# Kernel optimization log

Measured on AMD Instinct MI355X. Metric: run time of the kernel, lower is better.

## Reference

```python
import jax, jax.numpy as jnp
import numpy as np

N = 50000
HEADS1, HIM = 8, 16
NEG_SLOPE = 0.2


def gat_conv(x, src, dst, W, a_src, a_dst, bias, heads, out_dim, concat):
    n = x.shape[0]
    h = (x @ W).reshape(n, heads, out_dim)                      # [N,H,D]
    al_src = jnp.einsum('nhd,hd->nh', h, a_src)                  # [N,H]
    al_dst = jnp.einsum('nhd,hd->nh', h, a_dst)                  # [N,H]
    e = jax.nn.leaky_relu(al_src[src] + al_dst[dst], NEG_SLOPE)  # [E,H]
    # segment softmax over incoming edges of each destination node
    e_max = jax.ops.segment_max(e, dst, num_segments=n)
    e_max = jnp.where(jnp.isfinite(e_max), e_max, 0.0)
    ex = jnp.exp(e - e_max[dst])
    denom = jax.ops.segment_sum(ex, dst, num_segments=n)
    denom = jnp.where(denom == 0.0, 1.0, denom)
    alpha = ex / denom[dst]                                      # [E,H]
    msg = h[src] * alpha[:, :, None]                             # [E,H,D]
    out = jax.ops.segment_sum(msg, dst, num_segments=n)          # [N,H,D]
    out = out.reshape(n, heads * out_dim) if concat else out.mean(axis=1)
    return out + bias


def setup_inputs() -> dict:
    key = jax.random.key(0)
    ks = jax.random.split(key, 12)
    num_feature, out_feature, him = 128, 121, HIM
    E = 800000
    x = jax.random.normal(ks[0], (N, num_feature), dtype=jnp.float32)
    edge_index = jax.random.randint(ks[1], (2, E), 0, N, dtype=jnp.int64)
    s = 0.1
    W1 = jax.random.normal(ks[2], (num_feature, HEADS1 * him), dtype=jnp.float32) * s
    a_src1 = jax.random.normal(ks[3], (HEADS1, him), dtype=jnp.float32) * s
    a_dst1 = jax.random.normal(ks[4], (HEADS1, him), dtype=jnp.float32) * s
    b1 = jnp.zeros((HEADS1 * him,), dtype=jnp.float32)
    W2 = jax.random.normal(ks[5], (HEADS1 * him, out_feature), dtype=jnp.float32) * s
    a_src2 = jax.random.normal(ks[6], (1, out_feature), dtype=jnp.float32) * s
    a_dst2 = jax.random.normal(ks[7], (1, out_feature), dtype=jnp.float32) * s
    b2 = jnp.zeros((out_feature,), dtype=jnp.float32)
    return {"x": x, "edge_index": edge_index, "W1": W1, "a_src1": a_src1,
            "a_dst1": a_dst1, "b1": b1, "W2": W2, "a_src2": a_src2,
            "a_dst2": a_dst2, "b2": b2}


def reference(x, edge_index, W1, a_src1, a_dst1, b1, W2, a_src2, a_dst2, b2):
    n = x.shape[0]
    loops = jnp.arange(n, dtype=edge_index.dtype)
    src = jnp.concatenate([edge_index[0], loops])  # add self-loops (PyG default)
    dst = jnp.concatenate([edge_index[1], loops])
    h = gat_conv(x, src, dst, W1, a_src1, a_dst1, b1, HEADS1, HIM, True)
    h = jax.nn.relu(h)
    out = gat_conv(h, src, dst, W2, a_src2, a_dst2, b2, 1, W2.shape[1], True)
    return out
```

## Files before the change

kernel.cpp:

```cpp
#include <hip/hip_runtime.h>
#include <hip/hip_fp16.h>

#define NEG_SLOPE 0.2f

typedef __fp16 half8v __attribute__((ext_vector_type(8)));
typedef __fp16 half4v __attribute__((ext_vector_type(4)));
typedef float f32x4 __attribute__((ext_vector_type(4)));
typedef unsigned uint4u __attribute__((ext_vector_type(4), aligned(4)));
typedef float f32x4u __attribute__((ext_vector_type(4), aligned(4)));

__device__ __forceinline__ float lrelu(float x) {
    return fmaxf(x, 0.0f) + NEG_SLOPE * fminf(x, 0.0f);
}

__device__ __forceinline__ unsigned fkey(float f) {
    unsigned u = __float_as_uint(f);
    return (u & 0x80000000u) ? ~u : (u | 0x80000000u);
}
__device__ __forceinline__ float funkey(unsigned k) {
    return __uint_as_float((k & 0x80000000u) ? (k & 0x7fffffffu) : ~k);
}


__global__ __launch_bounds__(256) void scan_reduce(const int* __restrict__ cnt,
                                                   int* __restrict__ bsum, int n) {
    __shared__ int sm[256];
    int base = blockIdx.x * 1024 + threadIdx.x * 4;
    int s = 0;
#pragma unroll
    for (int j = 0; j < 4; ++j) {
        int i = base + j;
        if (i < n) s += cnt[i];
    }
    sm[threadIdx.x] = s;
    __syncthreads();
#pragma unroll
    for (int off = 128; off >= 1; off >>= 1) {
        if (threadIdx.x < off) sm[threadIdx.x] += sm[threadIdx.x + off];
        __syncthreads();
    }
    if (threadIdx.x == 0) bsum[blockIdx.x] = sm[0];
}

__global__ __launch_bounds__(256) void scan_bsum256(int* __restrict__ bsum, int nb) {
    __shared__ int sm[256];
    int v = (threadIdx.x < (unsigned)nb) ? bsum[threadIdx.x] : 0;
    sm[threadIdx.x] = v;
    __syncthreads();
    for (int off = 1; off < 256; off <<= 1) {
        int y = (threadIdx.x >= off) ? sm[threadIdx.x - off] : 0;
        __syncthreads();
        sm[threadIdx.x] += y;
        __syncthreads();
    }
    if (threadIdx.x < (unsigned)nb) bsum[threadIdx.x] = sm[threadIdx.x] - v;
}

__global__ __launch_bounds__(256) void scan_write(const int* __restrict__ cnt,
                                                  const int* __restrict__ bsum,
                                                  int* __restrict__ rp, int n) {
    __shared__ int sm[256];
    int base = blockIdx.x * 1024 + threadIdx.x * 4;
    int v[4];
    int s = 0;
#pragma unroll
    for (int j = 0; j < 4; ++j) {
        int i = base + j;
        v[j] = (i < n) ? cnt[i] : 0;
        s += v[j];
    }
    sm[threadIdx.x] = s;
    __syncthreads();
#pragma unroll
    for (int off = 1; off < 256; off <<= 1) {
        int y = (threadIdx.x >= off) ? sm[threadIdx.x - off] : 0;
        __syncthreads();
        sm[threadIdx.x] += y;
        __syncthreads();
    }
    int run = sm[threadIdx.x] - s + bsum[blockIdx.x];
#pragma unroll
    for (int j = 0; j < 4; ++j) {
        int i = base + j;
        if (i < n) {
            rp[i] = run;
            run += v[j];
            if (i == n - 1) rp[n] = run;
        }
    }
}


__global__ __launch_bounds__(256) void rhist1_kernel(const int* __restrict__ dst,
                                                     int* __restrict__ h, int E, int nblk) {
    __shared__ int lh[256];
    lh[threadIdx.x] = 0;
    __syncthreads();
    int base = blockIdx.x * 1024;
#pragma unroll
    for (int j = 0; j < 4; ++j) {
        int i = base + j * 256 + threadIdx.x;
        if (i < E) atomicAdd(&lh[dst[i] & 255], 1);
    }
    __syncthreads();
    h[threadIdx.x * nblk + blockIdx.x] = lh[threadIdx.x];
}

__global__ __launch_bounds__(256) void rhist2_kernel(const unsigned* __restrict__ kv,
                                                     int* __restrict__ h, int E, int nblk) {
    __shared__ int lh[256];
    lh[threadIdx.x] = 0;
    __syncthreads();
    int base = blockIdx.x * 1024;
#pragma unroll
    for (int j = 0; j < 4; ++j) {
        int i = base + j * 256 + threadIdx.x;
        if (i < E) atomicAdd(&lh[kv[i] >> 24], 1);
    }
    __syncthreads();
    h[threadIdx.x * nblk + blockIdx.x] = lh[threadIdx.x];
}

template <int SH, bool PACK>
__global__ __launch_bounds__(256) void rscat_kernel(const unsigned* __restrict__ in,
                                                    const int* __restrict__ srcp,
                                                    const int* __restrict__ dstp,
                                                    unsigned* __restrict__ outv,
                                                    const int* __restrict__ scanned,
                                                    int E, int nblk) {
    __shared__ unsigned items[1024];
    __shared__ unsigned sorted[1024];
    __shared__ int lh[256], lstart[256], rbase[256];
    __shared__ int wcnt[4][256];

    int tid = threadIdx.x, blk = blockIdx.x;
    int base = blk * 1024;
    int k = min(1024, E - base);
    lh[tid] = 0;
    rbase[tid] = 0;
#pragma unroll
    for (int j = 0; j < 4; ++j) {
        int idx = j * 256 + tid;
        unsigned v = 0u;
        if (base + idx < E) {
            if constexpr (PACK)
                v = ((unsigned)dstp[base + idx] << 16) | (unsigned)srcp[base + idx];
            else
                v = in[base + idx];
        }
        items[idx] = v;
    }
    __syncthreads();
#pragma unroll
    for (int j = 0; j < 4; ++j) {
        int idx = j * 256 + tid;
        if (idx < k) atomicAdd(&lh[(items[idx] >> SH) & 255], 1);
    }
    __syncthreads();
    int sv = lh[tid];
    lstart[tid] = sv;
    __syncthreads();
    for (int off = 1; off < 256; off <<= 1) {
        int y = (tid >= off) ? lstart[tid - off] : 0;
        __syncthreads();
        lstart[tid] += y;
        __syncthreads();
    }
    int excl = lstart[tid] - sv;
    __syncthreads();
    lstart[tid] = excl;
    __syncthreads();

    int lane = tid & 63, wave = tid >> 6;
#pragma unroll
    for (int it = 0; it < 4; ++it) {
        int idx = it * 256 + tid;
        unsigned v = items[idx];
        int d = (v >> SH) & 255;
        bool valid = idx < k;
        unsigned long long m = __ballot(valid);
#pragma unroll
        for (int b = 0; b < 8; ++b) {
            unsigned long long bb = __ballot((d >> b) & 1);
            m &= ((d >> b) & 1) ? bb : ~bb;
        }
        int lanerank = __popcll(m & ((1ull << lane) - 1ull));
        int wtot = __popcll(m);
        wcnt[0][tid] = 0; wcnt[1][tid] = 0; wcnt[2][tid] = 0; wcnt[3][tid] = 0;
        __syncthreads();
        if (valid && lanerank == 0) wcnt[wave][d] = wtot;
        __syncthreads();
        if (valid) {
            int cw = 0;
            for (int w = 0; w < wave; ++w) cw += wcnt[w][d];
            sorted[lstart[d] + rbase[d] + cw + lanerank] = v;
        }
        __syncthreads();
        rbase[tid] += wcnt[0][tid] + wcnt[1][tid] + wcnt[2][tid] + wcnt[3][tid];
        __syncthreads();
    }
#pragma unroll
    for (int j = 0; j < 4; ++j) {
        int i = j * 256 + tid;
        if (i < k) {
            unsigned v = sorted[i];
            int d = (v >> SH) & 255;
            outv[scanned[d * nblk + blk] + (i - lstart[d])] = v;
        }
    }
}


__global__ void rp_kernel(const unsigned* __restrict__ kv, int* __restrict__ rp,
                          int E, int N) {
    int i = blockIdx.x * 256 + threadIdx.x;
    if (i >= E) return;
    int cur = (int)(kv[i] >> 16);
    int prev = (i == 0) ? -1 : (int)(kv[i - 1] >> 16);
    for (int t = prev + 1; t <= cur; ++t) rp[t] = i;
    if (i == E - 1)
        for (int t = cur + 1; t <= N; ++t) rp[t] = E;
}


template <int H>
__global__ __launch_bounds__(256) void gmax_kernel(const float* __restrict__ a,
                                                   unsigned* __restrict__ gm, int total) {
    __shared__ unsigned sm[256];
    unsigned loc = 0;
    int stride = 256 * gridDim.x;
    for (int i = blockIdx.x * 256 + threadIdx.x; i < total; i += stride)
        loc = max(loc, fkey(a[i]));
    sm[threadIdx.x] = loc;
    __syncthreads();
    for (int off = 128; off >= H; off >>= 1) {
        if (threadIdx.x < off) sm[threadIdx.x] = max(sm[threadIdx.x], sm[threadIdx.x + off]);
        __syncthreads();
    }
    if (threadIdx.x < H) atomicMax(&gm[threadIdx.x], sm[threadIdx.x]);
}


__global__ __launch_bounds__(256) void w1_kernel(const unsigned* __restrict__ kv,
                                                 const float* __restrict__ alS,
                                                 const float* __restrict__ alD,
                                                 const unsigned* __restrict__ gm,
                                                 __half* __restrict__ w1t, int E) {
    int e = blockIdx.x * 256 + threadIdx.x;
    if (e >= E) return;
    unsigned k = kv[e];
    int s = (int)(k & 0xFFFFu), t = (int)(k >> 16);
    float sv[8], dv[8];
    *(f32x4*)&sv[0] = *(const f32x4*)(alS + (size_t)s * 8);
    *(f32x4*)&sv[4] = *(const f32x4*)(alS + (size_t)s * 8 + 4);
    *(f32x4*)&dv[0] = *(const f32x4*)(alD + (size_t)t * 8);
    *(f32x4*)&dv[4] = *(const f32x4*)(alD + (size_t)t * 8 + 4);
#pragma unroll
    for (int h = 0; h < 8; ++h) {
        float m = lrelu(funkey(gm[h]) + dv[h]);
        w1t[(size_t)h * E + e] = __float2half(__expf(lrelu(sv[h] + dv[h]) - m));
    }
}

__global__ void w2_kernel(const unsigned* __restrict__ kv, const float* __restrict__ alS,
                          const float* __restrict__ alD, const unsigned* __restrict__ gm,
                          float* __restrict__ w2v, int E) {
    int e = blockIdx.x * 256 + threadIdx.x;
    if (e >= E) return;
    unsigned k = kv[e];
    int s = (int)(k & 0xFFFFu), t = (int)(k >> 16);
    float adT = alD[t];
    w2v[e] = __expf(lrelu(alS[s] + adT) - lrelu(funkey(gm[0]) + adT));
}


template <int NC, typename AT, bool FUSE_AL2>
__global__ __launch_bounds__(256) void gemm_mfma(const AT* __restrict__ A,
                                                 const float* __restrict__ B,
                                                 __half* __restrict__ C, int M,
                                                 const float* __restrict__ as,
                                                 const float* __restrict__ ad,
                                                 float* __restrict__ alS,
                                                 float* __restrict__ alD) {
    __shared__ __half Bt[128][136];

    {
        int t = threadIdx.x;
        int c = t & 127;
        int kq = t >> 7;
#pragma unroll
        for (int ch = 0; ch < 8; ++ch) {
            int k0 = kq * 64 + ch * 8;
            half8v hv;
#pragma unroll
            for (int j = 0; j < 8; ++j) {
                float v = (c < NC) ? B[(size_t)(k0 + j) * NC + c] : 0.0f;
                hv[j] = (__fp16)v;
            }
            *(half8v*)&Bt[c][k0] = hv;
        }
    }
    __syncthreads();

    const int wid = threadIdx.x >> 6;
    const int lane = threadIdx.x & 63;
    const int li = lane & 15;
    const int lg = lane >> 4;

    int row = blockIdx.x * 64 + wid * 16 + li;
    int rowc = min(row, M - 1);

    half8v a[4];
#pragma unroll
    for (int ks = 0; ks < 4; ++ks) {
        int q = ks * 4 + lg;
        if constexpr (sizeof(AT) == 2) {
            a[ks] = *((const half8v*)(A + (size_t)rowc * 128) + q);
        } else {
            const float4* p = (const float4*)(A + (size_t)rowc * 128) + 2 * q;
            float4 a0 = p[0], a1 = p[1];
            half8v hv;
            hv[0] = (__fp16)a0.x; hv[1] = (__fp16)a0.y; hv[2] = (__fp16)a0.z; hv[3] = (__fp16)a0.w;
            hv[4] = (__fp16)a1.x; hv[5] = (__fp16)a1.y; hv[6] = (__fp16)a1.z; hv[7] = (__fp16)a1.w;
            a[ks] = hv;
        }
    }

    f32x4 acc[8];
#pragma unroll
    for (int ct = 0; ct < 8; ++ct) acc[ct] = (f32x4)0.0f;

#pragma unroll
    for (int ks = 0; ks < 4; ++ks) {
#pragma unroll
        for (int ct = 0; ct < 8; ++ct) {
            half8v b = *(const half8v*)&Bt[ct * 16 + li][ks * 32 + 8 * lg];
            acc[ct] = __builtin_amdgcn_mfma_f32_16x16x32_f16(a[ks], b, acc[ct], 0, 0, 0);
        }
    }

    int orow = blockIdx.x * 64 + wid * 16 + 4 * lg;
#pragma unroll
    for (int ct = 0; ct < 8; ++ct) {
#pragma unroll
        for (int r = 0; r < 4; ++r) {
            int rr = orow + r;
            if (rr < M) C[(size_t)rr * 128 + ct * 16 + li] = __float2half(acc[ct][r]);
        }
    }

    if constexpr (FUSE_AL2) {
        float asv[8], adv[8];
#pragma unroll
        for (int ct = 0; ct < 8; ++ct) {
            int c = ct * 16 + li;
            asv[ct] = (c < NC) ? as[c] : 0.0f;
            adv[ct] = (c < NC) ? ad[c] : 0.0f;
        }
#pragma unroll
        for (int r = 0; r < 4; ++r) {
            float s = 0.f, d = 0.f;
#pragma unroll
            for (int ct = 0; ct < 8; ++ct) {
                s = fmaf(acc[ct][r], asv[ct], s);
                d = fmaf(acc[ct][r], adv[ct], d);
            }
            s += __shfl_down(s, 8); d += __shfl_down(d, 8);
            s += __shfl_down(s, 4); d += __shfl_down(d, 4);
            s += __shfl_down(s, 2); d += __shfl_down(d, 2);
            s += __shfl_down(s, 1); d += __shfl_down(d, 1);
            if (li == 0) {
                int rr = orow + r;
                if (rr < M) { alS[rr] = s; alD[rr] = d; }
            }
        }
    }
}


__global__ void al1_kernel(const __half* __restrict__ h1h, const float* __restrict__ as,
                           const float* __restrict__ ad, float* __restrict__ alS,
                           float* __restrict__ alD, int N) {
    int g = blockIdx.x * 256 + threadIdx.x;
    if (g >= N * 8) return;
    int r = g >> 3, h = g & 7;
    const __half2* hp = (const __half2*)(h1h + (size_t)r * 128 + h * 16);
    const float* sp = as + h * 16;
    const float* dp = ad + h * 16;
    float s = 0.f, d = 0.f;
#pragma unroll
    for (int q = 0; q < 8; ++q) {
        float2 v = __half22float2(hp[q]);
        s = fmaf(v.x, sp[2 * q], s);
        d = fmaf(v.x, dp[2 * q], d);
        s = fmaf(v.y, sp[2 * q + 1], s);
        d = fmaf(v.y, dp[2 * q + 1], d);
    }
    alS[g] = s;
    alD[g] = d;
}


__global__ __launch_bounds__(256) void agg1_kernel(
    const __half* __restrict__ h1h, const float* __restrict__ alS,
    const float* __restrict__ alD, const float* __restrict__ b1,
    const int* __restrict__ rp, const unsigned* __restrict__ kv,
    const __half* __restrict__ w1t, const unsigned* __restrict__ gm,
    __half* __restrict__ h2h, int N, int E) {
    int t = blockIdx.x * 4 + (threadIdx.x >> 6);
    int lane = threadIdx.x & 63;
    int h = lane >> 3;

    float adh = alD[t * 8 + h];
    float mh = lrelu(funkey(gm[h]) + adh);
    int e0 = rp[t], e1 = rp[t + 1];

    float ex = __expf(lrelu(alS[t * 8 + h] + adh) - mh);
    float dsum = ex, dsum2 = 0.f;
    float2 hs = __half22float2(*(const __half2*)(h1h + (size_t)t * 128 + 2 * lane));
    float fx = ex * hs.x, fy = ex * hs.y;
    const __half* wrow = w1t + (size_t)h * E;

    int e = e0;
    while (e < e1 && (e & 3)) {
        int s0 = (int)(kv[e] & 0xFFFFu);
        float w0 = __half2float(wrow[e]);
        float2 f0 = __half22float2(*(const __half2*)(h1h + (size_t)s0 * 128 + 2 * lane));
        dsum2 += w0;
        fx = fmaf(w0, f0.x, fx); fy = fmaf(w0, f0.y, fy);
        ++e;
    }
    for (; e + 16 <= e1; e += 16) {
        uint4u kk[4];
        float ww[16];
#pragma unroll
        for (int q = 0; q < 4; ++q) {
            kk[q] = *(const uint4u*)&kv[e + 4 * q];
            half4v wv = *(const half4v*)&wrow[e + 4 * q];
#pragma unroll
            for (int r = 0; r < 4; ++r) ww[q * 4 + r] = (float)wv[r];
        }
        float2 ff[16];
#pragma unroll
        for (int q = 0; q < 4; ++q)
#pragma unroll
            for (int r = 0; r < 4; ++r)
                ff[q * 4 + r] = __half22float2(
                    *(const __half2*)(h1h + (size_t)(kk[q][r] & 0xFFFFu) * 128 + 2 * lane));
#pragma unroll
        for (int q = 0; q < 4; ++q) {
            if (q & 1) dsum2 += (ww[q * 4] + ww[q * 4 + 1]) + (ww[q * 4 + 2] + ww[q * 4 + 3]);
            else       dsum  += (ww[q * 4] + ww[q * 4 + 1]) + (ww[q * 4 + 2] + ww[q * 4 + 3]);
#pragma unroll
            for (int r = 0; r < 4; ++r) {
                float w = ww[q * 4 + r];
                float2 f = ff[q * 4 + r];
                fx = fmaf(w, f.x, fx);
                fy = fmaf(w, f.y, fy);
            }
        }
    }
    if (e + 8 <= e1) {
        uint4u ka = *(const uint4u*)&kv[e];
        uint4u kb = *(const uint4u*)&kv[e + 4];
        half4v wva = *(const half4v*)&wrow[e];
        half4v wvb = *(const half4v*)&wrow[e + 4];
        float2 f0 = __half22float2(*(const __half2*)(h1h + (size_t)(ka.x & 0xFFFFu) * 128 + 2 * lane));
        float2 f1 = __half22float2(*(const __half2*)(h1h + (size_t)(ka.y & 0xFFFFu) * 128 + 2 * lane));
        float2 f2 = __half22float2(*(const __half2*)(h1h + (size_t)(ka.z & 0xFFFFu) * 128 + 2 * lane));
        float2 f3 = __half22float2(*(const __half2*)(h1h + (size_t)(ka.w & 0xFFFFu) * 128 + 2 * lane));
        float2 f4 = __half22float2(*(const __half2*)(h1h + (size_t)(kb.x & 0xFFFFu) * 128 + 2 * lane));
        float2 f5 = __half22float2(*(const __half2*)(h1h + (size_t)(kb.y & 0xFFFFu) * 128 + 2 * lane));
        float2 f6 = __half22float2(*(const __half2*)(h1h + (size_t)(kb.z & 0xFFFFu) * 128 + 2 * lane));
        float2 f7 = __half22float2(*(const __half2*)(h1h + (size_t)(kb.w & 0xFFFFu) * 128 + 2 * lane));
        float w0 = (float)wva[0], w1 = (float)wva[1], w2 = (float)wva[2], w3 = (float)wva[3];
        float w4 = (float)wvb[0], w5 = (float)wvb[1], w6 = (float)wvb[2], w7 = (float)wvb[3];
        dsum += (w0 + w1) + (w2 + w3);
        dsum2 += (w4 + w5) + (w6 + w7);
        fx = fmaf(w0, f0.x, fx); fy = fmaf(w0, f0.y, fy);
        fx = fmaf(w1, f1.x, fx); fy = fmaf(w1, f1.y, fy);
        fx = fmaf(w2, f2.x, fx); fy = fmaf(w2, f2.y, fy);
        fx = fmaf(w3, f3.x, fx); fy = fmaf(w3, f3.y, fy);
        fx = fmaf(w4, f4.x, fx); fy = fmaf(w4, f4.y, fy);
        fx = fmaf(w5, f5.x, fx); fy = fmaf(w5, f5.y, fy);
        fx = fmaf(w6, f6.x, fx); fy = fmaf(w6, f6.y, fy);
        fx = fmaf(w7, f7.x, fx); fy = fmaf(w7, f7.y, fy);
        e += 8;
    }
    if (e + 4 <= e1) {
        uint4u ka = *(const uint4u*)&kv[e];
        half4v wva = *(const half4v*)&wrow[e];
        float2 f0 = __half22float2(*(const __half2*)(h1h + (size_t)(ka.x & 0xFFFFu) * 128 + 2 * lane));
        float2 f1 = __half22float2(*(const __half2*)(h1h + (size_t)(ka.y & 0xFFFFu) * 128 + 2 * lane));
        float2 f2 = __half22float2(*(const __half2*)(h1h + (size_t)(ka.z & 0xFFFFu) * 128 + 2 * lane));
        float2 f3 = __half22float2(*(const __half2*)(h1h + (size_t)(ka.w & 0xFFFFu) * 128 + 2 * lane));
        float w0 = (float)wva[0], w1 = (float)wva[1], w2 = (float)wva[2], w3 = (float)wva[3];
        dsum += (w0 + w1) + (w2 + w3);
        fx = fmaf(w0, f0.x, fx); fy = fmaf(w0, f0.y, fy);
        fx = fmaf(w1, f1.x, fx); fy = fmaf(w1, f1.y, fy);
        fx = fmaf(w2, f2.x, fx); fy = fmaf(w2, f2.y, fy);
        fx = fmaf(w3, f3.x, fx); fy = fmaf(w3, f3.y, fy);
        e += 4;
    }
    for (; e < e1; ++e) {
        int s0 = (int)(kv[e] & 0xFFFFu);
        float w0 = __half2float(wrow[e]);
        float2 f0 = __half22float2(*(const __half2*)(h1h + (size_t)s0 * 128 + 2 * lane));
        dsum2 += w0;
        fx = fmaf(w0, f0.x, fx); fy = fmaf(w0, f0.y, fy);
    }
    dsum += dsum2;
    float inv = 1.0f / dsum;
    float2 bb = *(const float2*)(b1 + 2 * lane);
    float ox = fmaxf(fmaf(fx, inv, bb.x), 0.0f);
    float oy = fmaxf(fmaf(fy, inv, bb.y), 0.0f);
    *(__half2*)(h2h + (size_t)t * 128 + 2 * lane) = __floats2half2_rn(ox, oy);
}


__global__ __launch_bounds__(256) void agg2_kernel(
    const __half* __restrict__ h3h, const float* __restrict__ alS,
    const float* __restrict__ alD, const float* __restrict__ b2,
    const int* __restrict__ rp, const unsigned* __restrict__ kv,
    const float* __restrict__ w2v, const unsigned* __restrict__ gm,
    float* __restrict__ out, int N, int NC) {
    int t = blockIdx.x * 4 + (threadIdx.x >> 6);
    int lane = threadIdx.x & 63;

    float adT = alD[t];
    float m = lrelu(funkey(gm[0]) + adT);
    int e0 = rp[t], e1 = rp[t + 1];

    float ex = __expf(lrelu(alS[t] + adT) - m);
    float dsum = ex, dsum2 = 0.f;
    float2 hs = __half22float2(*(const __half2*)(h3h + (size_t)t * 128 + 2 * lane));
    float fx = ex * hs.x, fy = ex * hs.y;

    int e = e0;
    for (; e + 16 <= e1; e += 16) {
        uint4u kk[4];
        f32x4u ww[4];
#pragma unroll
        for (int q = 0; q < 4; ++q) {
            kk[q] = *(const uint4u*)&kv[e + 4 * q];
            ww[q] = *(const f32x4u*)&w2v[e + 4 * q];
        }
        float2 ff[16];
#pragma unroll
        for (int q = 0; q < 4; ++q)
#pragma unroll
            for (int r = 0; r < 4; ++r)
                ff[q * 4 + r] = __half22float2(
                    *(const __half2*)(h3h + (size_t)(kk[q][r] & 0xFFFFu) * 128 + 2 * lane));
#pragma unroll
        for (int q = 0; q < 4; ++q) {
            if (q & 1) dsum2 += (ww[q][0] + ww[q][1]) + (ww[q][2] + ww[q][3]);
            else       dsum  += (ww[q][0] + ww[q][1]) + (ww[q][2] + ww[q][3]);
#pragma unroll
            for (int r = 0; r < 4; ++r) {
                float w = ww[q][r];
                float2 f = ff[q * 4 + r];
                fx = fmaf(w, f.x, fx);
                fy = fmaf(w, f.y, fy);
            }
        }
    }
    if (e + 8 <= e1) {
        uint4u ka = *(const uint4u*)&kv[e];
        uint4u kb = *(const uint4u*)&kv[e + 4];
        f32x4u wa = *(const f32x4u*)&w2v[e];
        f32x4u wb = *(const f32x4u*)&w2v[e + 4];
        float2 f0 = __half22float2(*(const __half2*)(h3h + (size_t)(ka.x & 0xFFFFu) * 128 + 2 * lane));
        float2 f1 = __half22float2(*(const __half2*)(h3h + (size_t)(ka.y & 0xFFFFu) * 128 + 2 * lane));
        float2 f2 = __half22float2(*(const __half2*)(h3h + (size_t)(ka.z & 0xFFFFu) * 128 + 2 * lane));
        float2 f3 = __half22float2(*(const __half2*)(h3h + (size_t)(ka.w & 0xFFFFu) * 128 + 2 * lane));
        float2 f4 = __half22float2(*(const __half2*)(h3h + (size_t)(kb.x & 0xFFFFu) * 128 + 2 * lane));
        float2 f5 = __half22float2(*(const __half2*)(h3h + (size_t)(kb.y & 0xFFFFu) * 128 + 2 * lane));
        float2 f6 = __half22float2(*(const __half2*)(h3h + (size_t)(kb.z & 0xFFFFu) * 128 + 2 * lane));
        float2 f7 = __half22float2(*(const __half2*)(h3h + (size_t)(kb.w & 0xFFFFu) * 128 + 2 * lane));
        dsum += (wa[0] + wa[1]) + (wa[2] + wa[3]);
        dsum2 += (wb[0] + wb[1]) + (wb[2] + wb[3]);
        fx = fmaf(wa[0], f0.x, fx); fy = fmaf(wa[0], f0.y, fy);
        fx = fmaf(wa[1], f1.x, fx); fy = fmaf(wa[1], f1.y, fy);
        fx = fmaf(wa[2], f2.x, fx); fy = fmaf(wa[2], f2.y, fy);
        fx = fmaf(wa[3], f3.x, fx); fy = fmaf(wa[3], f3.y, fy);
        fx = fmaf(wb[0], f4.x, fx); fy = fmaf(wb[0], f4.y, fy);
        fx = fmaf(wb[1], f5.x, fx); fy = fmaf(wb[1], f5.y, fy);
        fx = fmaf(wb[2], f6.x, fx); fy = fmaf(wb[2], f6.y, fy);
        fx = fmaf(wb[3], f7.x, fx); fy = fmaf(wb[3], f7.y, fy);
        e += 8;
    }
    if (e + 4 <= e1) {
        uint4u ka = *(const uint4u*)&kv[e];
        f32x4u wa = *(const f32x4u*)&w2v[e];
        float2 f0 = __half22float2(*(const __half2*)(h3h + (size_t)(ka.x & 0xFFFFu) * 128 + 2 * lane));
        float2 f1 = __half22float2(*(const __half2*)(h3h + (size_t)(ka.y & 0xFFFFu) * 128 + 2 * lane));
        float2 f2 = __half22float2(*(const __half2*)(h3h + (size_t)(ka.z & 0xFFFFu) * 128 + 2 * lane));
        float2 f3 = __half22float2(*(const __half2*)(h3h + (size_t)(ka.w & 0xFFFFu) * 128 + 2 * lane));
        dsum += (wa[0] + wa[1]) + (wa[2] + wa[3]);
        fx = fmaf(wa[0], f0.x, fx); fy = fmaf(wa[0], f0.y, fy);
        fx = fmaf(wa[1], f1.x, fx); fy = fmaf(wa[1], f1.y, fy);
        fx = fmaf(wa[2], f2.x, fx); fy = fmaf(wa[2], f2.y, fy);
        fx = fmaf(wa[3], f3.x, fx); fy = fmaf(wa[3], f3.y, fy);
        e += 4;
    }
    for (; e < e1; ++e) {
        int s0 = (int)(kv[e] & 0xFFFFu);
        float w0 = w2v[e];
        float2 f0 = __half22float2(*(const __half2*)(h3h + (size_t)s0 * 128 + 2 * lane));
        dsum2 += w0;
        fx = fmaf(w0, f0.x, fx); fy = fmaf(w0, f0.y, fy);
    }
    dsum += dsum2;
    float inv = 1.0f / dsum;
    int c0 = 2 * lane, c1 = 2 * lane + 1;
    if (c0 < NC) out[(size_t)t * NC + c0] = fmaf(fx, inv, b2[c0]);
    if (c1 < NC) out[(size_t)t * NC + c1] = fmaf(fy, inv, b2[c1]);
}


extern "C" void kernel_launch(void* const* d_in, const int* in_sizes, int n_in,
                              void* d_out, int out_size, void* d_ws, size_t ws_size,
                              hipStream_t stream) {
    const float* x   = (const float*)d_in[0];
    const int*   ei  = (const int*)d_in[1];
    const float* W1  = (const float*)d_in[2];
    const float* aS1 = (const float*)d_in[3];
    const float* aD1 = (const float*)d_in[4];
    const float* b1  = (const float*)d_in[5];
    const float* W2  = (const float*)d_in[6];
    const float* aS2 = (const float*)d_in[7];
    const float* aD2 = (const float*)d_in[8];
    const float* b2  = (const float*)d_in[9];
    float* out = (float*)d_out;

    const int N = in_sizes[0] / 128;
    const int E = in_sizes[1] / 2;
    const int NC2 = 121;

    const int NBLK = (E + 1023) / 1024;
    const int HN = 256 * NBLK;

    size_t off = 0;
    auto alloc = [&](size_t bytes) {
        size_t o = off;
        off = (off + bytes + 255) & ~(size_t)255;
        return o;
    };
    char* ws = (char*)d_ws;
    unsigned* kv0  = (unsigned*)(ws + alloc((size_t)E * 4));
    unsigned* kv1  = (unsigned*)(ws + alloc((size_t)E * 4));
    int*      h    = (int*)(ws + alloc((size_t)(HN + 1) * 4));
    int*      hs   = (int*)(ws + alloc((size_t)(HN + 1) * 4));
    int*      rp   = (int*)(ws + alloc((size_t)(N + 1) * 4));
    int*      bsum = (int*)(ws + alloc(256 * 4));
    float*    alS1 = (float*)(ws + alloc((size_t)N * 8 * 4));
    float*    alD1 = (float*)(ws + alloc((size_t)N * 8 * 4));
    float*    alS2 = (float*)(ws + alloc((size_t)N * 4));
    float*    alD2 = (float*)(ws + alloc((size_t)N * 4));
    unsigned* gm1  = (unsigned*)(ws + alloc(8 * 4));
    unsigned* gm2  = (unsigned*)(ws + alloc(4));
    __half*   w1t  = (__half*)(ws + alloc((size_t)E * 8 * 2));
    __half*   h1h  = (__half*)(ws + alloc((size_t)N * 128 * 2));
    __half*   h2h  = (__half*)(ws + alloc((size_t)N * 128 * 2));
    __half*   h3h  = h1h;
    float*    w2v  = (float*)kv1;
    if (ws_size < off) return;

    const int* src = ei;
    const int* dst = ei + E;

    hipMemsetAsync(gm1, 0, 8 * 4, stream);
    hipMemsetAsync(gm2, 0, 4, stream);

    int eb = (E + 255) / 256;
    int snb = (HN + 1023) / 1024;

    rhist1_kernel<<<NBLK, 256, 0, stream>>>(dst, h, E, NBLK);
    scan_reduce<<<snb, 256, 0, stream>>>(h, bsum, HN);
    scan_bsum256<<<1, 256, 0, stream>>>(bsum, snb);
    scan_write<<<snb, 256, 0, stream>>>(h, bsum, hs, HN);
    rscat_kernel<16, true><<<NBLK, 256, 0, stream>>>(nullptr, src, dst, kv1, hs, E, NBLK);
    rhist2_kernel<<<NBLK, 256, 0, stream>>>(kv1, h, E, NBLK);
    scan_reduce<<<snb, 256, 0, stream>>>(h, bsum, HN);
    scan_bsum256<<<1, 256, 0, stream>>>(bsum, snb);
    scan_write<<<snb, 256, 0, stream>>>(h, bsum, hs, HN);
    rscat_kernel<24, false><<<NBLK, 256, 0, stream>>>(kv1, nullptr, nullptr, kv0, hs, E, NBLK);
    rp_kernel<<<eb, 256, 0, stream>>>(kv0, rp, E, N);

    int gmb = (N + 63) / 64;
    int ab = (N + 3) / 4;
    gemm_mfma<128, float, false><<<gmb, 256, 0, stream>>>(x, W1, h1h, N,
                                                          nullptr, nullptr, nullptr, nullptr);
    al1_kernel<<<(N * 8 + 255) / 256, 256, 0, stream>>>(h1h, aS1, aD1, alS1, alD1, N);
    gmax_kernel<8><<<128, 256, 0, stream>>>(alS1, gm1, N * 8);
    w1_kernel<<<eb, 256, 0, stream>>>(kv0, alS1, alD1, gm1, w1t, E);
    agg1_kernel<<<ab, 256, 0, stream>>>(h1h, alS1, alD1, b1, rp, kv0, w1t, gm1, h2h, N, E);

    gemm_mfma<121, __half, true><<<gmb, 256, 0, stream>>>(h2h, W2, h3h, N,
                                                          aS2, aD2, alS2, alD2);
    gmax_kernel<1><<<128, 256, 0, stream>>>(alS2, gm2, N);
    w2_kernel<<<eb, 256, 0, stream>>>(kv0, alS2, alD2, gm2, w2v, E);
    agg2_kernel<<<ab, 256, 0, stream>>>(h3h, alS2, alD2, b2, rp, kv0, w2v, gm2, out, N, NC2);
}
```

Measured before the change: 200.8 us.

## Fuse al1/gmax/w1 and gmax2/w2 into cooperative kernels, merge scan passes

Replaces the separate al1, gmax and w1 kernels (and gmax/w2 for layer 2) with cooperative grid-synchronized kernels. Each one computes a per-block max, reduces it to a global max after a grid sync, then computes the edge weights. The scan's separate block-sum kernel is folded into scan_write2, where each block re-reduces the preceding block sums itself, and the memsets of the max buffers are dropped. This cuts kernel launches and inter-kernel gaps, at the cost of grid.sync overhead and a fixed 512-block cooperative grid.

```diff
diff --git a/kernel.cpp b/kernel.cpp
--- a/kernel.cpp
+++ b/kernel.cpp
@@ -1,5 +1,8 @@
 #include <hip/hip_runtime.h>
 #include <hip/hip_fp16.h>
+#include <hip/hip_cooperative_groups.h>
+
+namespace cg = cooperative_groups;
 
 #define NEG_SLOPE 0.2f
 
@@ -42,25 +45,24 @@
     if (threadIdx.x == 0) bsum[blockIdx.x] = sm[0];
 }
 
-__global__ __launch_bounds__(256) void scan_bsum256(int* __restrict__ bsum, int nb) {
+__global__ __launch_bounds__(256) void scan_write2(const int* __restrict__ cnt,
+                                                   const int* __restrict__ bsum,
+                                                   int* __restrict__ rp, int n) {
     __shared__ int sm[256];
-    int v = (threadIdx.x < (unsigned)nb) ? bsum[threadIdx.x] : 0;
-    sm[threadIdx.x] = v;
-    __syncthreads();
-    for (int off = 1; off < 256; off <<= 1) {
-        int y = (threadIdx.x >= off) ? sm[threadIdx.x - off] : 0;
-        __syncthreads();
-        sm[threadIdx.x] += y;
-        __syncthreads();
-    }
-    if (threadIdx.x < (unsigned)nb) bsum[threadIdx.x] = sm[threadIdx.x] - v;
-}
-
-__global__ __launch_bounds__(256) void scan_write(const int* __restrict__ cnt,
-                                                  const int* __restrict__ bsum,
-                                                  int* __restrict__ rp, int n) {
-    __shared__ int sm[256];
-    int base = blockIdx.x * 1024 + threadIdx.x * 4;
+    __shared__ int boff;
+    int tid = threadIdx.x;
+    int partial = (tid < blockIdx.x) ? bsum[tid] : 0;
+    sm[tid] = partial;
+    __syncthreads();
+#pragma unroll
+    for (int off = 128; off >= 1; off >>= 1) {
+        if (tid < off) sm[tid] += sm[tid + off];
+        __syncthreads();
+    }
+    if (tid == 0) boff = sm[0];
+    __syncthreads();
+
+    int base = blockIdx.x * 1024 + tid * 4;
     int v[4];
     int s = 0;
 #pragma unroll
@@ -69,16 +71,16 @@
         v[j] = (i < n) ? cnt[i] : 0;
         s += v[j];
     }
-    sm[threadIdx.x] = s;
+    sm[tid] = s;
     __syncthreads();
 #pragma unroll
     for (int off = 1; off < 256; off <<= 1) {
-        int y = (threadIdx.x >= off) ? sm[threadIdx.x - off] : 0;
-        __syncthreads();
-        sm[threadIdx.x] += y;
-        __syncthreads();
-    }
-    int run = sm[threadIdx.x] - s + bsum[blockIdx.x];
+        int y = (tid >= off) ? sm[tid - off] : 0;
+        __syncthreads();
+        sm[tid] += y;
+        __syncthreads();
+    }
+    int run = sm[tid] - s + boff;
 #pragma unroll
     for (int j = 0; j < 4; ++j) {
         int i = base + j;
@@ -223,54 +225,123 @@
 }
 
 
-template <int H>
-__global__ __launch_bounds__(256) void gmax_kernel(const float* __restrict__ a,
-                                                   unsigned* __restrict__ gm, int total) {
-    __shared__ unsigned sm[256];
+__global__ __launch_bounds__(256, 4) void al1_w1_fused(
+    const __half* __restrict__ h1h, const float* __restrict__ as,
+    const float* __restrict__ ad, float* __restrict__ alS, float* __restrict__ alD,
+    unsigned* __restrict__ bmax, unsigned* __restrict__ gm,
+    const unsigned* __restrict__ kv, __half* __restrict__ w1t, int N, int E) {
+    cg::grid_group grid = cg::this_grid();
+    __shared__ unsigned smu[256];
+    int tid = threadIdx.x;
+    int stride = gridDim.x * 256;
+
     unsigned loc = 0;
-    int stride = 256 * gridDim.x;
-    for (int i = blockIdx.x * 256 + threadIdx.x; i < total; i += stride)
-        loc = max(loc, fkey(a[i]));
-    sm[threadIdx.x] = loc;
-    __syncthreads();
-    for (int off = 128; off >= H; off >>= 1) {
-        if (threadIdx.x < off) sm[threadIdx.x] = max(sm[threadIdx.x], sm[threadIdx.x + off]);
-        __syncthreads();
-    }
-    if (threadIdx.x < H) atomicMax(&gm[threadIdx.x], sm[threadIdx.x]);
-}
-
-
-__global__ __launch_bounds__(256) void w1_kernel(const unsigned* __restrict__ kv,
-                                                 const float* __restrict__ alS,
-                                                 const float* __restrict__ alD,
-                                                 const unsigned* __restrict__ gm,
-                                                 __half* __restrict__ w1t, int E) {
-    int e = blockIdx.x * 256 + threadIdx.x;
-    if (e >= E) return;
-    unsigned k = kv[e];
-    int s = (int)(k & 0xFFFFu), t = (int)(k >> 16);
-    float sv[8], dv[8];
-    *(f32x4*)&sv[0] = *(const f32x4*)(alS + (size_t)s * 8);
-    *(f32x4*)&sv[4] = *(const f32x4*)(alS + (size_t)s * 8 + 4);
-    *(f32x4*)&dv[0] = *(const f32x4*)(alD + (size_t)t * 8);
-    *(f32x4*)&dv[4] = *(const f32x4*)(alD + (size_t)t * 8 + 4);
-#pragma unroll
-    for (int h = 0; h < 8; ++h) {
-        float m = lrelu(funkey(gm[h]) + dv[h]);
-        w1t[(size_t)h * E + e] = __float2half(__expf(lrelu(sv[h] + dv[h]) - m));
-    }
-}
-
-__global__ void w2_kernel(const unsigned* __restrict__ kv, const float* __restrict__ alS,
-                          const float* __restrict__ alD, const unsigned* __restrict__ gm,
-                          float* __restrict__ w2v, int E) {
-    int e = blockIdx.x * 256 + threadIdx.x;
-    if (e >= E) return;
-    unsigned k = kv[e];
-    int s = (int)(k & 0xFFFFu), t = (int)(k >> 16);
-    float adT = alD[t];
-    w2v[e] = __expf(lrelu(alS[s] + adT) - lrelu(funkey(gm[0]) + adT));
+    for (int g = blockIdx.x * 256 + tid; g < N * 8; g += stride) {
+        int r = g >> 3, h = g & 7;
+        const __half2* hp = (const __half2*)(h1h + (size_t)r * 128 + h * 16);
+        const float* sp = as + h * 16;
+        const float* dp = ad + h * 16;
+        float s = 0.f, d = 0.f;
+#pragma unroll
+        for (int q = 0; q < 8; ++q) {
+            float2 v = __half22float2(hp[q]);
+            s = fmaf(v.x, sp[2 * q], s);
+            d = fmaf(v.x, dp[2 * q], d);
+            s = fmaf(v.y, sp[2 * q + 1], s);
+            d = fmaf(v.y, dp[2 * q + 1], d);
+        }
+        alS[g] = s;
+        alD[g] = d;
+        loc = max(loc, fkey(s));
+    }
+    smu[tid] = loc;
+    __syncthreads();
+#pragma unroll
+    for (int off = 128; off >= 8; off >>= 1) {
+        if (tid < off) smu[tid] = max(smu[tid], smu[tid + off]);
+        __syncthreads();
+    }
+    if (tid < 8) bmax[blockIdx.x * 8 + tid] = smu[tid];
+    grid.sync();
+
+    if (blockIdx.x == 0) {
+        unsigned m = 0;
+        int total = gridDim.x * 8;
+        for (int i = tid; i < total; i += 256) m = max(m, bmax[i]);
+        smu[tid] = m;
+        __syncthreads();
+#pragma unroll
+        for (int off = 128; off >= 8; off >>= 1) {
+            if (tid < off) smu[tid] = max(smu[tid], smu[tid + off]);
+            __syncthreads();
+        }
+        if (tid < 8) gm[tid] = smu[tid];
+    }
+    grid.sync();
+
+    float gmv[8];
+#pragma unroll
+    for (int h = 0; h < 8; ++h) gmv[h] = funkey(gm[h]);
+
+    for (int e = blockIdx.x * 256 + tid; e < E; e += stride) {
+        unsigned k = kv[e];
+        int s = (int)(k & 0xFFFFu), t = (int)(k >> 16);
+        float sv[8], dv[8];
+        *(f32x4*)&sv[0] = *(const f32x4*)(alS + (size_t)s * 8);
+        *(f32x4*)&sv[4] = *(const f32x4*)(alS + (size_t)s * 8 + 4);
+        *(f32x4*)&dv[0] = *(const f32x4*)(alD + (size_t)t * 8);
+        *(f32x4*)&dv[4] = *(const f32x4*)(alD + (size_t)t * 8 + 4);
+#pragma unroll
+        for (int h = 0; h < 8; ++h) {
+            float m = lrelu(gmv[h] + dv[h]);
+            w1t[(size_t)h * E + e] = __float2half(__expf(lrelu(sv[h] + dv[h]) - m));
+        }
+    }
+}
+
+
+__global__ __launch_bounds__(256, 4) void gmax2_w2_fused(
+    const float* __restrict__ alS, const float* __restrict__ alD,
+    unsigned* __restrict__ bmax, unsigned* __restrict__ gm,
+    const unsigned* __restrict__ kv, float* __restrict__ w2v, int N, int E) {
+    cg::grid_group grid = cg::this_grid();
+    __shared__ unsigned smu[256];
+    int tid = threadIdx.x;
+    int stride = gridDim.x * 256;
+
+    unsigned loc = 0;
+    for (int i = blockIdx.x * 256 + tid; i < N; i += stride) loc = max(loc, fkey(alS[i]));
+    smu[tid] = loc;
+    __syncthreads();
+#pragma unroll
+    for (int off = 128; off >= 1; off >>= 1) {
+        if (tid < off) smu[tid] = max(smu[tid], smu[tid + off]);
+        __syncthreads();
+    }
+    if (tid == 0) bmax[blockIdx.x] = smu[0];
+    grid.sync();
+
+    if (blockIdx.x == 0) {
+        unsigned m = 0;
+        for (int i = tid; i < gridDim.x; i += 256) m = max(m, bmax[i]);
+        smu[tid] = m;
+        __syncthreads();
+#pragma unroll
+        for (int off = 128; off >= 1; off >>= 1) {
+            if (tid < off) smu[tid] = max(smu[tid], smu[tid + off]);
+            __syncthreads();
+        }
+        if (tid == 0) gm[0] = smu[0];
+    }
+    grid.sync();
+
+    float gmv = funkey(gm[0]);
+    for (int e = blockIdx.x * 256 + tid; e < E; e += stride) {
+        unsigned k = kv[e];
+        int s = (int)(k & 0xFFFFu), t = (int)(k >> 16);
+        float adT = alD[t];
+        w2v[e] = __expf(lrelu(alS[s] + adT) - lrelu(gmv + adT));
+    }
 }
 
 
@@ -375,29 +446,6 @@
             }
         }
     }
-}
-
-
-__global__ void al1_kernel(const __half* __restrict__ h1h, const float* __restrict__ as,
-                           const float* __restrict__ ad, float* __restrict__ alS,
-                           float* __restrict__ alD, int N) {
-    int g = blockIdx.x * 256 + threadIdx.x;
-    if (g >= N * 8) return;
-    int r = g >> 3, h = g & 7;
-    const __half2* hp = (const __half2*)(h1h + (size_t)r * 128 + h * 16);
-    const float* sp = as + h * 16;
-    const float* dp = ad + h * 16;
-    float s = 0.f, d = 0.f;
-#pragma unroll
-    for (int q = 0; q < 8; ++q) {
-        float2 v = __half22float2(hp[q]);
-        s = fmaf(v.x, sp[2 * q], s);
-        d = fmaf(v.x, dp[2 * q], d);
-        s = fmaf(v.y, sp[2 * q + 1], s);
-        d = fmaf(v.y, dp[2 * q + 1], d);
-    }
-    alS[g] = s;
-    alD[g] = d;
 }
 
 
@@ -640,6 +688,7 @@
 
     const int NBLK = (E + 1023) / 1024;
     const int HN = 256 * NBLK;
+    const int COOP = 512;
 
     size_t off = 0;
     auto alloc = [&](size_t bytes) {
@@ -651,18 +700,20 @@
     unsigned* kv0  = (unsigned*)(ws + alloc((size_t)E * 4));
     unsigned* kv1  = (unsigned*)(ws + alloc((size_t)E * 4));
     int*      h    = (int*)(ws + alloc((size_t)(HN + 1) * 4));
-    int*      hs   = (int*)(ws + alloc((size_t)(HN + 1) * 4));
+    int*      bsum = (int*)(ws + alloc(256 * 4));
     int*      rp   = (int*)(ws + alloc((size_t)(N + 1) * 4));
-    int*      bsum = (int*)(ws + alloc(256 * 4));
     float*    alS1 = (float*)(ws + alloc((size_t)N * 8 * 4));
     float*    alD1 = (float*)(ws + alloc((size_t)N * 8 * 4));
     float*    alS2 = (float*)(ws + alloc((size_t)N * 4));
     float*    alD2 = (float*)(ws + alloc((size_t)N * 4));
     unsigned* gm1  = (unsigned*)(ws + alloc(8 * 4));
     unsigned* gm2  = (unsigned*)(ws + alloc(4));
+    unsigned* bmax1 = (unsigned*)(ws + alloc((size_t)COOP * 8 * 4));
+    unsigned* bmax2 = (unsigned*)(ws + alloc((size_t)COOP * 4));
     __half*   w1t  = (__half*)(ws + alloc((size_t)E * 8 * 2));
     __half*   h1h  = (__half*)(ws + alloc((size_t)N * 128 * 2));
     __half*   h2h  = (__half*)(ws + alloc((size_t)N * 128 * 2));
+    int*      hs   = (int*)(ws + alloc((size_t)(HN + 1) * 4));
     __half*   h3h  = h1h;
     float*    w2v  = (float*)kv1;
     if (ws_size < off) return;
@@ -670,21 +721,16 @@
     const int* src = ei;
     const int* dst = ei + E;
 
-    hipMemsetAsync(gm1, 0, 8 * 4, stream);
-    hipMemsetAsync(gm2, 0, 4, stream);
-
     int eb = (E + 255) / 256;
     int snb = (HN + 1023) / 1024;
 
     rhist1_kernel<<<NBLK, 256, 0, stream>>>(dst, h, E, NBLK);
     scan_reduce<<<snb, 256, 0, stream>>>(h, bsum, HN);
-    scan_bsum256<<<1, 256, 0, stream>>>(bsum, snb);
-    scan_write<<<snb, 256, 0, stream>>>(h, bsum, hs, HN);
+    scan_write2<<<snb, 256, 0, stream>>>(h, bsum, hs, HN);
     rscat_kernel<16, true><<<NBLK, 256, 0, stream>>>(nullptr, src, dst, kv1, hs, E, NBLK);
     rhist2_kernel<<<NBLK, 256, 0, stream>>>(kv1, h, E, NBLK);
     scan_reduce<<<snb, 256, 0, stream>>>(h, bsum, HN);
-    scan_bsum256<<<1, 256, 0, stream>>>(bsum, snb);
-    scan_write<<<snb, 256, 0, stream>>>(h, bsum, hs, HN);
+    scan_write2<<<snb, 256, 0, stream>>>(h, bsum, hs, HN);
     rscat_kernel<24, false><<<NBLK, 256, 0, stream>>>(kv1, nullptr, nullptr, kv0, hs, E, NBLK);
     rp_kernel<<<eb, 256, 0, stream>>>(kv0, rp, E, N);
 
@@ -692,14 +738,24 @@
     int ab = (N + 3) / 4;
     gemm_mfma<128, float, false><<<gmb, 256, 0, stream>>>(x, W1, h1h, N,
                                                           nullptr, nullptr, nullptr, nullptr);
-    al1_kernel<<<(N * 8 + 255) / 256, 256, 0, stream>>>(h1h, aS1, aD1, alS1, alD1, N);
-    gmax_kernel<8><<<128, 256, 0, stream>>>(alS1, gm1, N * 8);
-    w1_kernel<<<eb, 256, 0, stream>>>(kv0, alS1, alD1, gm1, w1t, E);
+    {
+        int Nv = N, Ev = E;
+        void* args[] = {(void*)&h1h, (void*)&aS1, (void*)&aD1, (void*)&alS1, (void*)&alD1,
+                        (void*)&bmax1, (void*)&gm1, (void*)&kv0, (void*)&w1t,
+                        (void*)&Nv, (void*)&Ev};
+        hipLaunchCooperativeKernel((const void*)al1_w1_fused, dim3(COOP), dim3(256),
+                                   args, 0, stream);
+    }
     agg1_kernel<<<ab, 256, 0, stream>>>(h1h, alS1, alD1, b1, rp, kv0, w1t, gm1, h2h, N, E);
 
     gemm_mfma<121, __half, true><<<gmb, 256, 0, stream>>>(h2h, W2, h3h, N,
                                                           aS2, aD2, alS2, alD2);
-    gmax_kernel<1><<<128, 256, 0, stream>>>(alS2, gm2, N);
-    w2_kernel<<<eb, 256, 0, stream>>>(kv0, alS2, alD2, gm2, w2v, E);
+    {
+        int Nv = N, Ev = E;
+        void* args[] = {(void*)&alS2, (void*)&alD2, (void*)&bmax2, (void*)&gm2,
+                        (void*)&kv0, (void*)&w2v, (void*)&Nv, (void*)&Ev};
+        hipLaunchCooperativeKernel((const void*)gmax2_w2_fused, dim3(COOP), dim3(256),
+                                   args, 0, stream);
+    }
     agg2_kernel<<<ab, 256, 0, stream>>>(h3h, alS2, alD2, b2, rp, kv0, w2v, gm2, out, N, NC2);
 }
```

After: 389.5 us. 94.0% more time.
